# Performance work log

Hardware: AMD Instinct MI355X
Metric: run time of the kernel (lower is better)

The kernel has to match this reference:

```python
import jax, jax.numpy as jnp
import numpy as np

# Block-sparse linear config: W is (OUT_F, IN_F) in BSR form with BS x BS blocks,
OUT_F, IN_F, BS, K = 4096, 4096, 64, 32
NROW, NCOL = OUT_F // BS, IN_F // BS   # 64, 64
NNZB = NROW * K                         # 2048 nonzero blocks
BATCH = 8192


def setup_inputs() -> dict:
    key = jax.random.key(0)
    k1, k2, k3 = jax.random.split(key, 3)
    x = jax.random.normal(k1, (BATCH, IN_F), jnp.float32)
    values = jax.random.normal(k2, (NNZB, BS, BS), jnp.float32) * 0.02
    bias = jax.random.normal(k3, (OUT_F,), jnp.float32) * 0.01
    # BSR structure: K sorted, distinct column-block indices per block-row.
    cols = np.stack([np.sort((r + 2 * np.arange(K)) % NCOL) for r in range(NROW)])
    col_indices = jnp.asarray(cols.reshape(-1), jnp.int32)          # [NNZB]
    crow_indices = jnp.arange(NROW + 1, dtype=jnp.int32) * K        # [NROW+1]
    return {"x": x, "values": values, "bias": bias,
            "crow_indices": crow_indices, "col_indices": col_indices}


def reference(x, values, bias, crow_indices, col_indices):
    # Expand BSR row pointers to per-block row ids (structure is static/int).
    counts = jnp.diff(crow_indices)
    row_ids = jnp.repeat(jnp.arange(NROW), counts, total_repeat_length=NNZB)
    # Scatter nonzero blocks into a dense weight (only ~67 MB, cheap vs the GEMM).
    Wb = jnp.zeros((NROW, NCOL, BS, BS), values.dtype).at[row_ids, col_indices].set(values)
    W = Wb.transpose(0, 2, 1, 3).reshape(OUT_F, IN_F)  # [out_features, in_features]
    # forward: (W @ x.T).T + bias  ==  x @ W.T + bias
    return x @ W.T + bias
```

## Files before the change

kernel.cpp:

```cpp
#include <hip/hip_runtime.h>
#include <stdint.h>


#define BATCH   8192
#define IN_F    4096
#define OUT_F   4096
#define BS      64
#define BK      32
#define NROW    64
#define NNZB    2048
#define BM      256
#define LDS_A_BYTES (BM * BK * 2)
#define LDS_B_BYTES (2 * BS * BK * 2)
#define BUF_BYTES   (LDS_A_BYTES + LDS_B_BYTES)
#define NBUF    2

typedef float f32x4 __attribute__((ext_vector_type(4)));
typedef short s16x8 __attribute__((ext_vector_type(8)));

__device__ __forceinline__ void async_copy16(const void* g, void* l) {
  __builtin_amdgcn_global_load_lds(
      (__attribute__((address_space(1))) void*)g,
      (__attribute__((address_space(3))) void*)l, 16, 0, 0);
}

__device__ __forceinline__ unsigned short f32_to_bf16(float f) {
  union { float f; uint32_t u; } v; v.f = f;
  return (unsigned short)((v.u + 0x7FFFu + ((v.u >> 16) & 1u)) >> 16);
}

__global__ void cvt_kernel(const float4* __restrict__ xin,
                           const float4* __restrict__ win,
                           ushort4* __restrict__ xout,
                           ushort4* __restrict__ wout, int nx4, int ntot4) {
  int i = blockIdx.x * blockDim.x + threadIdx.x;
  if (i >= ntot4) return;
  const float4* src; ushort4* dst; int j;
  if (i < nx4) { src = xin; dst = xout; j = i; }
  else         { src = win; dst = wout; j = i - nx4; }
  float4 v = src[j];
  ushort4 o;
  o.x = f32_to_bf16(v.x); o.y = f32_to_bf16(v.y);
  o.z = f32_to_bf16(v.z); o.w = f32_to_bf16(v.w);
  dst[j] = o;
}

__global__ __launch_bounds__(512) void bsr_gemm_pair_kernel(
    const unsigned short* __restrict__ xb,
    const unsigned short* __restrict__ wb,
    const float* __restrict__ bias,
    const int* __restrict__ crow,
    const int* __restrict__ cols,
    float* __restrict__ out) {
  __shared__ alignas(16) char smem[NBUF * BUF_BYTES];

  const int tid = threadIdx.x;
  const int w   = tid >> 6;
  const int l   = tid & 63;
  const int wm  = w & 3;
  const int wn  = w >> 2;
  const int p   = blockIdx.x;
  const int rA  = ((p >> 1) << 2) + (p & 1);
  const int rB  = rA + 2;
  const int m0  = blockIdx.y * BM;

  const int startA = crow[rA], endA = crow[rA + 1];
  const int startB = crow[rB], endB = crow[rB + 1];

  const int lr = l & 15;
  const int q  = l >> 4;

  int cvA = (startA + l < endA) ? cols[startA + l] : 0;
  int cvB = (startB + l < endB) ? cols[startB + l] : 0;

  int myc = 0, mypk = 0;
  int nt = 0;
  {
    int ia = startA, ib = startB;
    const int clA = (endA > startA) ? endA - 1 : 0;
    const int clB = (endB > startB) ? endB - 1 : 0;
    while ((ia < endA) || (ib < endB)) {
      const int ca = (ia < endA) ? __shfl(cvA, ia - startA) : 0x7fffffff;
      const int cb = (ib < endB) ? __shfl(cvB, ib - startB) : 0x7fffffff;
      const int c  = min(ca, cb);
      const int hA = (ca == c);
      const int hB = (cb == c);
      const int sA = hA ? ia : clA;
      const int sB = hB ? ib : clB;
      if (nt == l) { myc = c; mypk = sA | (sB << 12) | (hA << 24) | (hB << 25); }
      ia += hA; ib += hB; ++nt;
    }
  }

  f32x4 acc[4][4];
#pragma unroll
  for (int mi = 0; mi < 4; ++mi)
#pragma unroll
    for (int ni = 0; ni < 4; ++ni) {
      f32x4 z = {0.f, 0.f, 0.f, 0.f};
      acc[mi][ni] = z;
    }

  const int swz8 = (((tid & 3) ^ ((tid >> 3) & 3)) << 3);
  const unsigned short* agbase =
      xb + (size_t)(m0 + (tid >> 2)) * IN_F + swz8;
  const int bgoff = (((tid & 255) >> 2) << 6) + swz8;
  const int bblk = tid >> 8;

  auto stage = [&](int h, int buf) {
    const int t  = h >> 1;
    const int k0 = (h & 1) << 5;
    const int c  = __shfl(myc, t);
    const int pk = __shfl(mypk, t);
    const int sA = pk & 0xfff;
    const int sB = (pk >> 12) & 0xfff;
    char* const al = smem + buf * BUF_BYTES + tid * 16;
    char* const bl = smem + buf * BUF_BYTES + LDS_A_BYTES + tid * 16;
    const unsigned short* ag = agbase + (size_t)c * BS + k0;
    async_copy16(ag, al);
    async_copy16(ag + (size_t)128 * IN_F, al + 8192);
    const int sblk = bblk ? sB : sA;
    async_copy16(wb + ((size_t)sblk << 12) + bgoff + k0, bl);
  };

  const int nh = nt << 1;
  if (nh > 0) stage(0, 0);
  __syncthreads();
  int cur = 0;
  for (int h = 0; h < nh; ++h) {
    if (h + 1 < nh) stage(h + 1, cur ^ 1);

    const int pk = __shfl(mypk, h >> 1);
    const char* const cbase = smem + cur * BUF_BYTES;
    if ((pk >> (24 + wn)) & 1) {
      __builtin_amdgcn_s_setprio(1);
      const int chunk = ((q ^ ((lr >> 1) & 3)) << 4);
      s16x8 af[4], bf[4];
#pragma unroll
      for (int mi = 0; mi < 4; ++mi)
        af[mi] = *(const s16x8*)(cbase +
                   ((wm << 6) + (mi << 4) + lr) * 64 + chunk);
#pragma unroll
      for (int ni = 0; ni < 4; ++ni)
        bf[ni] = *(const s16x8*)(cbase + LDS_A_BYTES + (wn << 12) +
                   ((ni << 4) + lr) * 64 + chunk);
#pragma unroll
      for (int mi = 0; mi < 4; ++mi)
#pragma unroll
        for (int ni = 0; ni < 4; ++ni)
          acc[mi][ni] = __builtin_amdgcn_mfma_f32_16x16x32_bf16(
              af[mi], bf[ni], acc[mi][ni], 0, 0, 0);
      __builtin_amdgcn_s_setprio(0);
    }
    __syncthreads();
    cur ^= 1;
  }

  const int rW = wn ? rB : rA;
  const int colg = (rW << 6) + lr;
#pragma unroll
  for (int ni = 0; ni < 4; ++ni) {
    const float bv = bias[colg + (ni << 4)];
#pragma unroll
    for (int mi = 0; mi < 4; ++mi) {
      float* op = out +
          (size_t)(m0 + (wm << 6) + (mi << 4) + (q << 2)) * OUT_F +
          colg + (ni << 4);
#pragma unroll
      for (int e = 0; e < 4; ++e)
        op[(size_t)e * OUT_F] = acc[mi][ni][e] + bv;
    }
  }
}

__global__ void fallback_kernel(const float* __restrict__ x,
                                const float* __restrict__ vals,
                                const float* __restrict__ bias,
                                const int* __restrict__ crow,
                                const int* __restrict__ cols,
                                float* __restrict__ out) {
  int idx = blockIdx.x * 256 + threadIdx.x;
  int m = idx >> 12;
  int n = idx & 4095;
  int r = n >> 6, nl = n & 63;
  float s = 0.f;
  int e = crow[r + 1];
  for (int i = crow[r]; i < e; ++i) {
    const float* xp = x + (size_t)m * IN_F + cols[i] * 64;
    const float* wp = vals + ((size_t)i << 12) + nl * 64;
    for (int k = 0; k < 64; ++k) s += xp[k] * wp[k];
  }
  out[idx] = s + bias[n];
}

extern "C" void kernel_launch(void* const* d_in, const int* in_sizes, int n_in,
                              void* d_out, int out_size, void* d_ws,
                              size_t ws_size, hipStream_t stream) {
  const float* x    = (const float*)d_in[0];
  const float* vals = (const float*)d_in[1];
  const float* bias = (const float*)d_in[2];
  const int*   crow = (const int*)d_in[3];
  const int*   cols = (const int*)d_in[4];
  float* out = (float*)d_out;

  const size_t x_elems = (size_t)BATCH * IN_F;
  const size_t w_elems = (size_t)NNZB * BS * BS;
  const size_t need = (x_elems + w_elems) * 2;

  if (ws_size >= need) {
    unsigned short* xb = (unsigned short*)d_ws;
    unsigned short* wbp = xb + x_elems;
    const int nx4 = (int)(x_elems / 4);
    const int ntot4 = (int)((x_elems + w_elems) / 4);
    cvt_kernel<<<(ntot4 + 255) / 256, 256, 0, stream>>>(
        (const float4*)x, (const float4*)vals,
        (ushort4*)xb, (ushort4*)wbp, nx4, ntot4);
    dim3 grid(NROW / 2, BATCH / BM);
    bsr_gemm_pair_kernel<<<grid, 512, 0, stream>>>(xb, wbp, bias, crow, cols,
                                                   out);
  } else {
    fallback_kernel<<<(BATCH * OUT_F) / 256, 256, 0, stream>>>(
        x, vals, bias, crow, cols, out);
  }
}
```

Baseline: 388.5 us.

## Use 256-thread blocks with 128x64 warp tiles and triple-buffered async loads

Halves the block to 4 waves so each wave computes an 8x4 grid of MFMA tiles (128 rows by 64 columns), doubling register accumulators and data reuse per LDS fragment. The LDS pipeline moves from double to triple buffering: each step waits with an explicit vmcnt and a raw s_barrier instead of __syncthreads, so loads for step h+2 overlap compute on step h. Each thread now issues 6 async copies per stage instead of 3. The change trades higher register pressure and more LDS per block (about 72 KB) for fewer barriers and deeper prefetch, and may reduce occupancy.

```diff
diff --git a/kernel.cpp b/kernel.cpp
--- a/kernel.cpp
+++ b/kernel.cpp
@@ -13,7 +13,7 @@
 #define LDS_A_BYTES (BM * BK * 2)
 #define LDS_B_BYTES (2 * BS * BK * 2)
 #define BUF_BYTES   (LDS_A_BYTES + LDS_B_BYTES)
-#define NBUF    2
+#define NBUF    3
 
 typedef float f32x4 __attribute__((ext_vector_type(4)));
 typedef short s16x8 __attribute__((ext_vector_type(8)));
@@ -45,7 +45,7 @@
   dst[j] = o;
 }
 
-__global__ __launch_bounds__(512) void bsr_gemm_pair_kernel(
+__global__ __launch_bounds__(256, 2) void bsr_gemm_pair_kernel(
     const unsigned short* __restrict__ xb,
     const unsigned short* __restrict__ wb,
     const float* __restrict__ bias,
@@ -57,8 +57,8 @@
   const int tid = threadIdx.x;
   const int w   = tid >> 6;
   const int l   = tid & 63;
-  const int wm  = w & 3;
-  const int wn  = w >> 2;
+  const int wm  = w & 1;
+  const int wn  = w >> 1;
   const int p   = blockIdx.x;
   const int rA  = ((p >> 1) << 2) + (p & 1);
   const int rB  = rA + 2;
@@ -92,9 +92,9 @@
     }
   }
 
-  f32x4 acc[4][4];
-#pragma unroll
-  for (int mi = 0; mi < 4; ++mi)
+  f32x4 acc[8][4];
+#pragma unroll
+  for (int mi = 0; mi < 8; ++mi)
 #pragma unroll
     for (int ni = 0; ni < 4; ++ni) {
       f32x4 z = {0.f, 0.f, 0.f, 0.f};
@@ -104,8 +104,9 @@
   const int swz8 = (((tid & 3) ^ ((tid >> 3) & 3)) << 3);
   const unsigned short* agbase =
       xb + (size_t)(m0 + (tid >> 2)) * IN_F + swz8;
-  const int bgoff = (((tid & 255) >> 2) << 6) + swz8;
-  const int bblk = tid >> 8;
+  const int bgoff = ((tid >> 2) << 6) + swz8;
+  char* const alds = smem + tid * 16;
+  char* const blds = smem + LDS_A_BYTES + tid * 16;
 
   auto stage = [&](int h, int buf) {
     const int t  = h >> 1;
@@ -114,46 +115,55 @@
     const int pk = __shfl(mypk, t);
     const int sA = pk & 0xfff;
     const int sB = (pk >> 12) & 0xfff;
-    char* const al = smem + buf * BUF_BYTES + tid * 16;
-    char* const bl = smem + buf * BUF_BYTES + LDS_A_BYTES + tid * 16;
+    char* const al = alds + buf * BUF_BYTES;
+    char* const bl = blds + buf * BUF_BYTES;
     const unsigned short* ag = agbase + (size_t)c * BS + k0;
-    async_copy16(ag, al);
-    async_copy16(ag + (size_t)128 * IN_F, al + 8192);
-    const int sblk = bblk ? sB : sA;
-    async_copy16(wb + ((size_t)sblk << 12) + bgoff + k0, bl);
+#pragma unroll
+    for (int it = 0; it < 4; ++it)
+      async_copy16(ag + (size_t)(it * 64) * IN_F, al + it * 4096);
+    async_copy16(wb + ((size_t)sA << 12) + bgoff + k0, bl);
+    async_copy16(wb + ((size_t)sB << 12) + bgoff + k0, bl + 4096);
   };
 
   const int nh = nt << 1;
   if (nh > 0) stage(0, 0);
-  __syncthreads();
-  int cur = 0;
+  if (nh > 1) stage(1, 1);
+  int cur = 0, nx2 = 2;
   for (int h = 0; h < nh; ++h) {
-    if (h + 1 < nh) stage(h + 1, cur ^ 1);
+    if (h + 1 < nh) {
+      asm volatile("s_waitcnt vmcnt(6)" ::: "memory");
+    } else {
+      asm volatile("s_waitcnt vmcnt(0)" ::: "memory");
+    }
+    __builtin_amdgcn_s_barrier();
+    __builtin_amdgcn_sched_barrier(0);
+
+    if (h + 2 < nh) stage(h + 2, nx2);
 
     const int pk = __shfl(mypk, h >> 1);
     const char* const cbase = smem + cur * BUF_BYTES;
     if ((pk >> (24 + wn)) & 1) {
       __builtin_amdgcn_s_setprio(1);
       const int chunk = ((q ^ ((lr >> 1) & 3)) << 4);
-      s16x8 af[4], bf[4];
-#pragma unroll
-      for (int mi = 0; mi < 4; ++mi)
+      s16x8 af[8], bf[4];
+#pragma unroll
+      for (int mi = 0; mi < 8; ++mi)
         af[mi] = *(const s16x8*)(cbase +
-                   ((wm << 6) + (mi << 4) + lr) * 64 + chunk);
+                   ((wm << 7) + (mi << 4) + lr) * 64 + chunk);
 #pragma unroll
       for (int ni = 0; ni < 4; ++ni)
         bf[ni] = *(const s16x8*)(cbase + LDS_A_BYTES + (wn << 12) +
                    ((ni << 4) + lr) * 64 + chunk);
 #pragma unroll
-      for (int mi = 0; mi < 4; ++mi)
+      for (int mi = 0; mi < 8; ++mi)
 #pragma unroll
         for (int ni = 0; ni < 4; ++ni)
           acc[mi][ni] = __builtin_amdgcn_mfma_f32_16x16x32_bf16(
               af[mi], bf[ni], acc[mi][ni], 0, 0, 0);
       __builtin_amdgcn_s_setprio(0);
     }
-    __syncthreads();
-    cur ^= 1;
+    cur = (cur == 2) ? 0 : cur + 1;
+    nx2 = (nx2 == 2) ? 0 : nx2 + 1;
   }
 
   const int rW = wn ? rB : rA;
@@ -162,9 +172,9 @@
   for (int ni = 0; ni < 4; ++ni) {
     const float bv = bias[colg + (ni << 4)];
 #pragma unroll
-    for (int mi = 0; mi < 4; ++mi) {
+    for (int mi = 0; mi < 8; ++mi) {
       float* op = out +
-          (size_t)(m0 + (wm << 6) + (mi << 4) + (q << 2)) * OUT_F +
+          (size_t)(m0 + (wm << 7) + (mi << 4) + (q << 2)) * OUT_F +
           colg + (ni << 4);
 #pragma unroll
       for (int e = 0; e < 4; ++e)
@@ -216,7 +226,7 @@
         (const float4*)x, (const float4*)vals,
         (ushort4*)xb, (ushort4*)wbp, nx4, ntot4);
     dim3 grid(NROW / 2, BATCH / BM);
-    bsr_gemm_pair_kernel<<<grid, 512, 0, stream>>>(xb, wbp, bias, crow, cols,
+    bsr_gemm_pair_kernel<<<grid, 256, 0, stream>>>(xb, wbp, bias, crow, cols,
                                                    out);
   } else {
     fallback_kernel<<<(BATCH * OUT_F) / 256, 256, 0, stream>>>(
```

Result: no change. 393.3 us (+1.2%).
